# Optimization experiments

Hardware: AMD Instinct MI355X
Metric: run time of the kernel (lower is better)

Reference implementation:

```python
import jax, jax.numpy as jnp
import numpy as np

N = 50000
E = 800000
D = 128
L = 2
EPS = 1e-12  # BatchNorm1d eps in the module
NEG_SLOPE = 0.2  # PyG GATConv default leaky_relu slope


def setup_inputs() -> dict:
    key = jax.random.key(0)
    ks = jax.random.split(key, 12)
    x = jax.random.normal(ks[0], (N, D), dtype=jnp.float32)
    # edges guaranteed non-self (GATConv removes then re-adds self loops)
    src = jax.random.randint(ks[1], (E,), 0, N)
    off = jax.random.randint(ks[2], (E,), 1, N)
    dst = (src + off) % N
    edge_index = jnp.stack([src, dst]).astype(jnp.int64)
    scale = 1.0 / np.sqrt(D)
    Ws = jax.random.normal(ks[3], (L, D, D), dtype=jnp.float32) * scale
    a_src = jax.random.normal(ks[4], (L, D), dtype=jnp.float32) * scale
    a_dst = jax.random.normal(ks[5], (L, D), dtype=jnp.float32) * scale
    bias = jax.random.normal(ks[6], (L, D), dtype=jnp.float32) * 0.01
    gamma = jnp.ones((L, D), dtype=jnp.float32)
    beta = jnp.zeros((L, D), dtype=jnp.float32)
    run_mean = jax.random.normal(ks[7], (L, D), dtype=jnp.float32) * 0.01
    run_var = jax.random.uniform(ks[8], (L, D), minval=0.5, maxval=1.5, dtype=jnp.float32)
    return {"x": x, "edge_index": edge_index, "Ws": Ws, "a_src": a_src,
            "a_dst": a_dst, "bias": bias, "gamma": gamma, "beta": beta,
            "run_mean": run_mean, "run_var": run_var}


def _gat_layer(x, src, dst, W, asrc, adst, b):
    # x: [N, d_in]; W: [d_in, D]
    h = x @ W  # [N, D]
    e = jnp.take(h @ asrc, src) + jnp.take(h @ adst, dst)  # [E'] per-edge score
    e = jnp.where(e > 0, e, NEG_SLOPE * e)  # leaky_relu
    # segment softmax over destination node
    m = jax.ops.segment_max(e, dst, num_segments=N)
    ee = jnp.exp(e - jnp.take(m, dst))
    s = jax.ops.segment_sum(ee, dst, num_segments=N)
    alpha = ee / jnp.take(s, dst)
    # scatter-aggregate weighted source features
    msg = alpha[:, None] * jnp.take(h, src, axis=0)  # [E', D]
    out = jax.ops.segment_sum(msg, dst, num_segments=N)
    return out + b


def reference(x, edge_index, Ws, a_src, a_dst, bias, gamma, beta, run_mean, run_var):
    src, dst = edge_index[0], edge_index[1]
    # GATConv add_self_loops=True
    loops = jnp.arange(N, dtype=src.dtype)
    src = jnp.concatenate([src, loops])
    dst = jnp.concatenate([dst, loops])
    for i in range(L):
        x = _gat_layer(x, src, dst, Ws[i], a_src[i], a_dst[i], bias[i])
        # BatchNorm1d (eval mode, running stats) + ReLU
        x = (x - run_mean[i]) * (gamma[i] * jax.lax.rsqrt(run_var[i] + EPS)) + beta[i]
        x = jax.nn.relu(x)
    return x
```

## Files before the change

kernel.cpp:

```cpp
#include <hip/hip_runtime.h>

constexpr int Dd = 128;
constexpr float BN_EPS = 1e-12f;
constexpr float NEG_SLOPE = 0.2f;

using bf16x8 = __attribute__((ext_vector_type(8))) short;
using f32x4  = __attribute__((ext_vector_type(4))) float;

__device__ __forceinline__ ushort f2bf(float f) {
    unsigned u = __float_as_uint(f);
    return (ushort)((u + 0x7fffu + ((u >> 16) & 1u)) >> 16);
}
__device__ __forceinline__ float lrelu(float x) { return x > 0.f ? x : NEG_SLOPE * x; }

__global__ __launch_bounds__(256) void wprep_zero_kernel(
    const float* __restrict__ W, ushort* __restrict__ Wt, int* __restrict__ cntc,
    const float* __restrict__ bias, const float* __restrict__ gamma,
    const float* __restrict__ beta, const float* __restrict__ mean,
    const float* __restrict__ var, float* __restrict__ kA, float* __restrict__ kB)
{
    int t = threadIdx.x;
    if (blockIdx.x >= 2) {
        cntc[t] = 0;
        float sc = gamma[t] * rsqrtf(var[t] + BN_EPS);
        kA[t] = sc;
        kB[t] = (bias[t] - mean[t]) * sc + beta[t];
        return;
    }
    __shared__ float lds[32][33];
    const float* Wl = W + (size_t)blockIdx.x * Dd * Dd;
    ushort* Wo = Wt + (size_t)blockIdx.x * Dd * Dd;
    int r = t >> 3, c4 = (t & 7) << 2;
    for (int tk = 0; tk < 4; ++tk)
    for (int tn = 0; tn < 4; ++tn) {
        int k0 = tk * 32, n0 = tn * 32;
        float4 v = *(const float4*)&Wl[(size_t)(k0 + r) * Dd + n0 + c4];
        lds[r][c4] = v.x; lds[r][c4 + 1] = v.y; lds[r][c4 + 2] = v.z; lds[r][c4 + 3] = v.w;
        __syncthreads();
        ushort4 o;
        o.x = f2bf(lds[c4 + 0][r]); o.y = f2bf(lds[c4 + 1][r]);
        o.z = f2bf(lds[c4 + 2][r]); o.w = f2bf(lds[c4 + 3][r]);
        *(ushort4*)&Wo[(size_t)(n0 + r) * Dd + k0 + c4] = o;
        __syncthreads();
    }
}

__global__ __launch_bounds__(256) void coarse_hist_kernel(
    const int* __restrict__ dst, int* __restrict__ cntc, int E, int NB)
{
    __shared__ int lh[256];
    int t = threadIdx.x;
    lh[t] = 0;
    __syncthreads();
    for (int e = blockIdx.x * 256 + t; e < E; e += gridDim.x * 256)
        atomicAdd(&lh[dst[e] >> 8], 1);
    __syncthreads();
    if (t < NB && lh[t]) atomicAdd(&cntc[t], lh[t]);
}

__global__ __launch_bounds__(256) void coarse_scan_kernel(
    const int* __restrict__ cntc, int* __restrict__ base,
    int* __restrict__ cursor, int NB, int E)
{
    __shared__ int lds[256];
    int t = threadIdx.x;
    int v0 = (t < NB) ? cntc[t] : 0;
    lds[t] = v0;
    __syncthreads();
    for (int o = 1; o < 256; o <<= 1) {
        int v = (t >= o) ? lds[t - o] : 0;
        __syncthreads();
        lds[t] += v;
        __syncthreads();
    }
    int excl = lds[t] - v0;
    if (t < NB) { base[t] = excl; cursor[t] = excl; }
    if (t == 0) base[NB] = E;
}

__global__ __launch_bounds__(256) void partition_kernel(
    const int* __restrict__ src, const int* __restrict__ dst,
    int* __restrict__ cursor, unsigned* __restrict__ gpart, int E)
{
    __shared__ int h[256], lb[256], gs[256], cur[256];
    __shared__ unsigned staged[4096];
    const int t = threadIdx.x;
    const int c0 = blockIdx.x * 4096;
    const int count = min(4096, E - c0);

    h[t] = 0; cur[t] = 0;
    __syncthreads();
#pragma unroll
    for (int j = 0; j < 16; ++j) {
        int idx = j * 256 + t;
        if (idx < count) atomicAdd(&h[dst[c0 + idx] >> 8], 1);
    }
    __syncthreads();
    {
        int v0 = h[t];
        lb[t] = v0;
        __syncthreads();
        for (int o = 1; o < 256; o <<= 1) {
            int v = (t >= o) ? lb[t - o] : 0;
            __syncthreads();
            lb[t] += v;
            __syncthreads();
        }
        lb[t] -= v0;
    }
    if (h[t]) gs[t] = atomicAdd(&cursor[t], h[t]);
    __syncthreads();
#pragma unroll
    for (int j = 0; j < 16; ++j) {
        int idx = j * 256 + t;
        if (idx < count) {
            int d = dst[c0 + idx], s = src[c0 + idx];
            int b = d >> 8;
            int pos = lb[b] + atomicAdd(&cur[b], 1);
            staged[pos] = (unsigned)s | ((unsigned)(d & 255) << 16) | ((unsigned)b << 24);
        }
    }
    __syncthreads();
#pragma unroll
    for (int j = 0; j < 16; ++j) {
        int idx = j * 256 + t;
        if (idx < count) {
            unsigned p = staged[idx];
            int b = p >> 24;
            gpart[gs[b] + (idx - lb[b])] = p;
        }
    }
}

__global__ __launch_bounds__(256) void bucket_csr_kernel(
    const unsigned* __restrict__ gpart, const int* __restrict__ base,
    int* __restrict__ rowptr, int* __restrict__ ssrc, int N, int NB, int Etot)
{
    __shared__ int h[256], lb[256], cur[256];
    const int t = threadIdx.x;
    const int b = blockIdx.x;
    const int cb = base[b], ce = base[b + 1];
    const int cb2 = cb + b * 256;
    const int cnt = ce - cb;

    h[t] = 0; cur[t] = 0;
    __syncthreads();
    for (int o = t; o < cnt; o += 256)
        atomicAdd(&h[(gpart[cb + o] >> 16) & 255], 1);
    __syncthreads();
    {
        int v0 = h[t];
        lb[t] = v0;
        __syncthreads();
        for (int o = 1; o < 256; o <<= 1) {
            int v = (t >= o) ? lb[t - o] : 0;
            __syncthreads();
            lb[t] += v;
            __syncthreads();
        }
        lb[t] -= v0;
    }
    int n0 = b * 256 + t;
    if (n0 < N) {
        int rp = cb2 + lb[t] + t;
        rowptr[n0] = rp;
        ssrc[rp] = n0;
    }
    if (b == 0 && t == 0) rowptr[N] = Etot;
    __syncthreads();
    for (int o = t; o < cnt; o += 256) {
        unsigned p = gpart[cb + o];
        int n = (p >> 16) & 255;
        int pos = lb[n] + atomicAdd(&cur[n], 1);
        ssrc[cb2 + pos + n + 1] = (int)(p & 0xFFFFu);
    }
}

template<bool BF16IN>
__global__ __launch_bounds__(256) void gemm_mfma(
    const void* __restrict__ Xv, const ushort* __restrict__ Wt,
    const float* __restrict__ asrc, const float* __restrict__ adst,
    _Float16* __restrict__ Hf, float* __restrict__ hs, float* __restrict__ hd, int N)
{
    __shared__ ushort Xs[64 * 128];
    __shared__ ushort Bs[128 * 128];

    const int t = threadIdx.x;
    const int lane = t & 63, wid = t >> 6;
    const int row0 = blockIdx.x * 64;

    if constexpr (BF16IN) {
        const ushort* X = (const ushort*)Xv;
#pragma unroll
        for (int p = 0; p < 4; ++p) {
            int id = t + p * 256;
            int r = id >> 4, b16 = id & 15;
            int g = row0 + r;
            uint4 v = make_uint4(0, 0, 0, 0);
            if (g < N) v = *(const uint4*)&X[(size_t)g * Dd + b16 * 8];
            *(uint4*)&Xs[r * 128 + ((b16 ^ (r & 15)) << 3)] = v;
        }
    } else {
        const float* X = (const float*)Xv;
#pragma unroll
        for (int p = 0; p < 8; ++p) {
            int id = t + p * 256;
            int r = id >> 5, c4g = id & 31;
            int g = row0 + r;
            float4 v = make_float4(0.f, 0.f, 0.f, 0.f);
            if (g < N) v = *(const float4*)&X[(size_t)g * Dd + c4g * 4];
            ushort4 o; o.x = f2bf(v.x); o.y = f2bf(v.y); o.z = f2bf(v.z); o.w = f2bf(v.w);
            int b16 = c4g >> 1, sub = c4g & 1;
            *(ushort4*)&Xs[r * 128 + (((b16 ^ (r & 15)) << 3) | (sub << 2))] = o;
        }
    }
#pragma unroll
    for (int p = 0; p < 8; ++p) {
        int id = t + p * 256;
        int n = id >> 4, b16 = id & 15;
        uint4 v = *(const uint4*)&Wt[(size_t)n * 128 + b16 * 8];
        *(uint4*)&Bs[n * 128 + ((b16 ^ (n & 15)) << 3)] = v;
    }
    __syncthreads();

    f32x4 acc[8];
#pragma unroll
    for (int f = 0; f < 8; ++f) acc[f] = (f32x4){0.f, 0.f, 0.f, 0.f};

#pragma unroll
    for (int kk = 0; kk < 4; ++kk) {
        int ra = wid * 16 + (lane & 15);
        int b16 = (lane >> 4) + kk * 4;
        bf16x8 a = *(bf16x8*)&Xs[ra * 128 + ((b16 ^ (ra & 15)) << 3)];
#pragma unroll
        for (int f = 0; f < 8; ++f) {
            int nb = f * 16 + (lane & 15);
            bf16x8 b = *(bf16x8*)&Bs[nb * 128 + ((b16 ^ (nb & 15)) << 3)];
            acc[f] = __builtin_amdgcn_mfma_f32_16x16x32_bf16(a, b, acc[f], 0, 0, 0);
        }
    }

    float aS[8], aD[8];
#pragma unroll
    for (int f = 0; f < 8; ++f) {
        aS[f] = asrc[(lane & 15) + f * 16];
        aD[f] = adst[(lane & 15) + f * 16];
    }
#pragma unroll
    for (int j = 0; j < 4; ++j) {
        int r = row0 + wid * 16 + (lane >> 4) * 4 + j;
        float ps = 0.f, pd = 0.f;
#pragma unroll
        for (int f = 0; f < 8; ++f) { ps += acc[f][j] * aS[f]; pd += acc[f][j] * aD[f]; }
#pragma unroll
        for (int o = 8; o; o >>= 1) { ps += __shfl_xor(ps, o); pd += __shfl_xor(pd, o); }
        if (r < N) {
#pragma unroll
            for (int f = 0; f < 8; ++f)
                Hf[(size_t)r * Dd + (lane & 15) + f * 16] = (_Float16)acc[f][j];
            if ((lane & 15) == 0) { hs[r] = ps; hd[r] = pd; }
        }
    }
}

template<bool BF16OUT>
__global__ __launch_bounds__(256) void gat_agg_kernel(
    const int* __restrict__ rowptr, const int* __restrict__ ssrc,
    const float* __restrict__ hs, const float* __restrict__ hd,
    const _Float16* __restrict__ Hf,
    const float* __restrict__ kA, const float* __restrict__ kB,
    void* __restrict__ outv, int N)
{
    const int wid = (blockIdx.x * 256 + threadIdx.x) >> 6;
    if (wid >= N) return;
    const int lane = threadIdx.x & 63;
    const int q = lane >> 4, li = lane & 15;
    const size_t rowO = (size_t)wid * Dd;

    const float hdi = hd[wid];
    float acc[8];
#pragma unroll
    for (int m = 0; m < 8; ++m) acc[m] = 0.f;
    float s = 0.f;

    const int rs = rowptr[wid];
    const int nv = rowptr[wid + 1] - rs;

    union HU { uint4 u; _Float16 h[8]; };
    HU r0, r1; r0.u = make_uint4(0,0,0,0); r1.u = make_uint4(0,0,0,0);
    float h0 = 0.f, h1 = 0.f;
    if (q < nv) {
        int sj = ssrc[rs + q];
        h0 = hs[sj];
        r0.u = *(const uint4*)&Hf[(size_t)sj * Dd + li * 8];
    }
    if (4 + q < nv) {
        int sj = ssrc[rs + 4 + q];
        h1 = hs[sj];
        r1.u = *(const uint4*)&Hf[(size_t)sj * Dd + li * 8];
    }

    const int nit = (nv + 3) >> 2;
    for (int it = 0; it < nit; ++it) {
        float scv = h0 + hdi;
        scv = scv > 0.f ? scv : NEG_SLOPE * scv;
        float ee = (it * 4 + q < nv) ? __expf(scv) : 0.f;
        s += ee;
        HU rc = r0;
        r0 = r1; h0 = h1;
        int pn = (it + 2) * 4 + q;
        if (pn < nv) {
            int sj = ssrc[rs + pn];
            h1 = hs[sj];
            r1.u = *(const uint4*)&Hf[(size_t)sj * Dd + li * 8];
        }
#pragma unroll
        for (int m = 0; m < 8; ++m)
            acc[m] = fmaf((float)rc.h[m], ee, acc[m]);
    }

#pragma unroll
    for (int m = 0; m < 8; ++m) {
        acc[m] += __shfl_xor(acc[m], 16);
        acc[m] += __shfl_xor(acc[m], 32);
    }
    s += __shfl_xor(s, 16);
    s += __shfl_xor(s, 32);

    if (q == 0) {
        float inv = 1.0f / s;
        int c0 = li * 8;
        float4 ka0 = *(const float4*)&kA[c0],     ka1 = *(const float4*)&kA[c0 + 4];
        float4 kb0 = *(const float4*)&kB[c0],     kb1 = *(const float4*)&kB[c0 + 4];
        float o[8];
        o[0] = fmaxf(acc[0] * inv * ka0.x + kb0.x, 0.f);
        o[1] = fmaxf(acc[1] * inv * ka0.y + kb0.y, 0.f);
        o[2] = fmaxf(acc[2] * inv * ka0.z + kb0.z, 0.f);
        o[3] = fmaxf(acc[3] * inv * ka0.w + kb0.w, 0.f);
        o[4] = fmaxf(acc[4] * inv * ka1.x + kb1.x, 0.f);
        o[5] = fmaxf(acc[5] * inv * ka1.y + kb1.y, 0.f);
        o[6] = fmaxf(acc[6] * inv * ka1.z + kb1.z, 0.f);
        o[7] = fmaxf(acc[7] * inv * ka1.w + kb1.w, 0.f);
        if constexpr (BF16OUT) {
            ushort* out = (ushort*)outv;
            uint4 pk;
#pragma unroll
            for (int k = 0; k < 4; ++k)
                ((unsigned*)&pk)[k] = (unsigned)f2bf(o[2 * k]) | ((unsigned)f2bf(o[2 * k + 1]) << 16);
            *(uint4*)&out[rowO + c0] = pk;
        } else {
            float* out = (float*)outv;
            *(float4*)&out[rowO + c0]     = make_float4(o[0], o[1], o[2], o[3]);
            *(float4*)&out[rowO + c0 + 4] = make_float4(o[4], o[5], o[6], o[7]);
        }
    }
}

extern "C" void kernel_launch(void* const* d_in, const int* in_sizes, int n_in,
                              void* d_out, int out_size, void* d_ws, size_t ws_size,
                              hipStream_t stream)
{
    const float* x     = (const float*)d_in[0];
    const int*   ei    = (const int*)d_in[1];
    const float* Ws    = (const float*)d_in[2];
    const float* a_src = (const float*)d_in[3];
    const float* a_dst = (const float*)d_in[4];
    const float* bias  = (const float*)d_in[5];
    const float* gamma = (const float*)d_in[6];
    const float* beta  = (const float*)d_in[7];
    const float* mean  = (const float*)d_in[8];
    const float* var   = (const float*)d_in[9];
    float* out = (float*)d_out;
    float* ws  = (float*)d_ws;

    const int N = in_sizes[0] / Dd;
    const int E = in_sizes[1] / 2;
    const int Etot = E + N;
    const int NB = (N + 255) >> 8;
    const int* src = ei;
    const int* dst = ei + E;

    float*    hs   = ws;
    float*    hd   = hs + N;
    _Float16* Hf   = (_Float16*)(hd + N);
    ushort*   xmid = (ushort*)(Hf + (size_t)N * Dd);
    ushort*   WtB  = xmid + (size_t)N * Dd;
    float*    kAB  = (float*)(WtB + 2 * Dd * Dd);
    int* rowptr  = (int*)(kAB + 512);
    int* cntc    = rowptr + (N + 1);
    int* base    = cntc + 256;
    int* cursor  = base + 257;
    unsigned* gpart = (unsigned*)(cursor + 256);
    int* ssrc    = (int*)(gpart + E);

    const int gemm_blocks = (N + 63) / 64;
    const int part_blocks = (E + 4095) / 4096;
    const int agg_blocks  = (N * 64 + 255) / 256;

    wprep_zero_kernel<<<3, 256, 0, stream>>>(Ws, WtB, cntc, bias, gamma, beta, mean, var,
                                             kAB, kAB + 256);
    coarse_hist_kernel<<<256, 256, 0, stream>>>(dst, cntc, E, NB);
    coarse_scan_kernel<<<1, 256, 0, stream>>>(cntc, base, cursor, NB, E);
    partition_kernel<<<part_blocks, 256, 0, stream>>>(src, dst, cursor, gpart, E);
    bucket_csr_kernel<<<NB, 256, 0, stream>>>(gpart, base, rowptr, ssrc, N, NB, Etot);

    for (int l = 0; l < 2; ++l) {
        const float* kA_l = kAB + l * 128;
        const float* kB_l = kAB + 256 + l * 128;

        if (l == 0)
            gemm_mfma<false><<<gemm_blocks, 256, 0, stream>>>(
                (const void*)x, WtB, a_src, a_dst, Hf, hs, hd, N);
        else
            gemm_mfma<true><<<gemm_blocks, 256, 0, stream>>>(
                (const void*)xmid, WtB + (size_t)Dd * Dd, a_src + Dd, a_dst + Dd, Hf, hs, hd, N);

        if (l == 0)
            gat_agg_kernel<true><<<agg_blocks, 256, 0, stream>>>(
                rowptr, ssrc, hs, hd, Hf, kA_l, kB_l, (void*)xmid, N);
        else
            gat_agg_kernel<false><<<agg_blocks, 256, 0, stream>>>(
                rowptr, ssrc, hs, hd, Hf, kA_l, kB_l, (void*)out, N);
    }
}
```

Baseline: 242.7 us.

## Fuse layer-0 GEMM with degree histogram and deepen aggregation prefetch

The coarse destination histogram now runs as extra blocks of the layer-0 GEMM launch. This removes one kernel launch and lets the histogram overlap with the GEMM, since neither depends on the other. The aggregation loop now prefetches four neighbor groups ahead instead of two, via an unrolled rotating-register macro, to hide gather latency. The cost is more registers per thread, which may lower occupancy.

```diff
diff --git a/kernel.cpp b/kernel.cpp
--- a/kernel.cpp
+++ b/kernel.cpp
@@ -45,19 +45,6 @@
     }
 }
 
-__global__ __launch_bounds__(256) void coarse_hist_kernel(
-    const int* __restrict__ dst, int* __restrict__ cntc, int E, int NB)
-{
-    __shared__ int lh[256];
-    int t = threadIdx.x;
-    lh[t] = 0;
-    __syncthreads();
-    for (int e = blockIdx.x * 256 + t; e < E; e += gridDim.x * 256)
-        atomicAdd(&lh[dst[e] >> 8], 1);
-    __syncthreads();
-    if (t < NB && lh[t]) atomicAdd(&cntc[t], lh[t]);
-}
-
 __global__ __launch_bounds__(256) void coarse_scan_kernel(
     const int* __restrict__ cntc, int* __restrict__ base,
     int* __restrict__ cursor, int NB, int E)
@@ -176,9 +163,92 @@
     }
 }
 
-template<bool BF16IN>
-__global__ __launch_bounds__(256) void gemm_mfma(
-    const void* __restrict__ Xv, const ushort* __restrict__ Wt,
+__global__ __launch_bounds__(256) void gemm0_hist_kernel(
+    const float* __restrict__ X, const ushort* __restrict__ Wt,
+    const float* __restrict__ asrc, const float* __restrict__ adst,
+    _Float16* __restrict__ Hf, float* __restrict__ hs, float* __restrict__ hd, int N,
+    int nGemm, const int* __restrict__ dst, int* __restrict__ cntc, int E, int NB)
+{
+    const int t = threadIdx.x;
+    if (blockIdx.x >= nGemm) {
+        __shared__ int lh[256];
+        lh[t] = 0;
+        __syncthreads();
+        const int nb = 256;
+        for (int e = (blockIdx.x - nGemm) * 256 + t; e < E; e += nb * 256)
+            atomicAdd(&lh[dst[e] >> 8], 1);
+        __syncthreads();
+        if (t < NB && lh[t]) atomicAdd(&cntc[t], lh[t]);
+        return;
+    }
+
+    __shared__ ushort Xs[64 * 128];
+    __shared__ ushort Bs[128 * 128];
+    const int lane = t & 63, wid = t >> 6;
+    const int row0 = blockIdx.x * 64;
+
+#pragma unroll
+    for (int p = 0; p < 8; ++p) {
+        int id = t + p * 256;
+        int r = id >> 5, c4g = id & 31;
+        int g = row0 + r;
+        float4 v = make_float4(0.f, 0.f, 0.f, 0.f);
+        if (g < N) v = *(const float4*)&X[(size_t)g * Dd + c4g * 4];
+        ushort4 o; o.x = f2bf(v.x); o.y = f2bf(v.y); o.z = f2bf(v.z); o.w = f2bf(v.w);
+        int b16 = c4g >> 1, sub = c4g & 1;
+        *(ushort4*)&Xs[r * 128 + (((b16 ^ (r & 15)) << 3) | (sub << 2))] = o;
+    }
+#pragma unroll
+    for (int p = 0; p < 8; ++p) {
+        int id = t + p * 256;
+        int n = id >> 4, b16 = id & 15;
+        uint4 v = *(const uint4*)&Wt[(size_t)n * 128 + b16 * 8];
+        *(uint4*)&Bs[n * 128 + ((b16 ^ (n & 15)) << 3)] = v;
+    }
+    __syncthreads();
+
+    f32x4 acc[8];
+#pragma unroll
+    for (int f = 0; f < 8; ++f) acc[f] = (f32x4){0.f, 0.f, 0.f, 0.f};
+
+#pragma unroll
+    for (int kk = 0; kk < 4; ++kk) {
+        int ra = wid * 16 + (lane & 15);
+        int b16 = (lane >> 4) + kk * 4;
+        bf16x8 a = *(bf16x8*)&Xs[ra * 128 + ((b16 ^ (ra & 15)) << 3)];
+#pragma unroll
+        for (int f = 0; f < 8; ++f) {
+            int nb2 = f * 16 + (lane & 15);
+            bf16x8 b = *(bf16x8*)&Bs[nb2 * 128 + ((b16 ^ (nb2 & 15)) << 3)];
+            acc[f] = __builtin_amdgcn_mfma_f32_16x16x32_bf16(a, b, acc[f], 0, 0, 0);
+        }
+    }
+
+    float aS[8], aD[8];
+#pragma unroll
+    for (int f = 0; f < 8; ++f) {
+        aS[f] = asrc[(lane & 15) + f * 16];
+        aD[f] = adst[(lane & 15) + f * 16];
+    }
+#pragma unroll
+    for (int j = 0; j < 4; ++j) {
+        int r = row0 + wid * 16 + (lane >> 4) * 4 + j;
+        float ps = 0.f, pd = 0.f;
+#pragma unroll
+        for (int f = 0; f < 8; ++f) { ps += acc[f][j] * aS[f]; pd += acc[f][j] * aD[f]; }
+#pragma unroll
+        for (int o = 8; o; o >>= 1) { ps += __shfl_xor(ps, o); pd += __shfl_xor(pd, o); }
+        if (r < N) {
+#pragma unroll
+            for (int f = 0; f < 8; ++f)
+                Hf[(size_t)r * Dd + (lane & 15) + f * 16] = (_Float16)acc[f][j];
+            if ((lane & 15) == 0) { hs[r] = ps; hd[r] = pd; }
+        }
+    }
+}
+
+__global__ __launch_bounds__(256) void gemm_mfma_bf16(
+    const ushort* __restrict__ X, const ushort* __restrict__ Wt,
     const float* __restrict__ asrc, const float* __restrict__ adst,
     _Float16* __restrict__ Hf, float* __restrict__ hs, float* __restrict__ hd, int N)
 {
@@ -189,30 +259,14 @@
     const int lane = t & 63, wid = t >> 6;
     const int row0 = blockIdx.x * 64;
 
-    if constexpr (BF16IN) {
-        const ushort* X = (const ushort*)Xv;
-#pragma unroll
-        for (int p = 0; p < 4; ++p) {
-            int id = t + p * 256;
-            int r = id >> 4, b16 = id & 15;
-            int g = row0 + r;
-            uint4 v = make_uint4(0, 0, 0, 0);
-            if (g < N) v = *(const uint4*)&X[(size_t)g * Dd + b16 * 8];
-            *(uint4*)&Xs[r * 128 + ((b16 ^ (r & 15)) << 3)] = v;
-        }
-    } else {
-        const float* X = (const float*)Xv;
-#pragma unroll
-        for (int p = 0; p < 8; ++p) {
-            int id = t + p * 256;
-            int r = id >> 5, c4g = id & 31;
-            int g = row0 + r;
-            float4 v = make_float4(0.f, 0.f, 0.f, 0.f);
-            if (g < N) v = *(const float4*)&X[(size_t)g * Dd + c4g * 4];
-            ushort4 o; o.x = f2bf(v.x); o.y = f2bf(v.y); o.z = f2bf(v.z); o.w = f2bf(v.w);
-            int b16 = c4g >> 1, sub = c4g & 1;
-            *(ushort4*)&Xs[r * 128 + (((b16 ^ (r & 15)) << 3) | (sub << 2))] = o;
-        }
+#pragma unroll
+    for (int p = 0; p < 4; ++p) {
+        int id = t + p * 256;
+        int r = id >> 4, b16 = id & 15;
+        int g = row0 + r;
+        uint4 v = make_uint4(0, 0, 0, 0);
+        if (g < N) v = *(const uint4*)&X[(size_t)g * Dd + b16 * 8];
+        *(uint4*)&Xs[r * 128 + ((b16 ^ (r & 15)) << 3)] = v;
     }
 #pragma unroll
     for (int p = 0; p < 8; ++p) {
@@ -287,37 +341,45 @@
     const int nv = rowptr[wid + 1] - rs;
 
     union HU { uint4 u; _Float16 h[8]; };
-    HU r0, r1; r0.u = make_uint4(0,0,0,0); r1.u = make_uint4(0,0,0,0);
-    float h0 = 0.f, h1 = 0.f;
-    if (q < nv) {
-        int sj = ssrc[rs + q];
-        h0 = hs[sj];
-        r0.u = *(const uint4*)&Hf[(size_t)sj * Dd + li * 8];
-    }
-    if (4 + q < nv) {
-        int sj = ssrc[rs + 4 + q];
-        h1 = hs[sj];
-        r1.u = *(const uint4*)&Hf[(size_t)sj * Dd + li * 8];
-    }
+    HU r0, r1, r2, r3;
+    r0.u = r1.u = r2.u = r3.u = make_uint4(0, 0, 0, 0);
+    float h0 = 0.f, h1 = 0.f, h2 = 0.f, h3 = 0.f;
+
+    if (q < nv)      { int sj = ssrc[rs + q];      h0 = hs[sj]; r0.u = *(const uint4*)&Hf[(size_t)sj * Dd + li * 8]; }
+    if (4 + q < nv)  { int sj = ssrc[rs + 4 + q];  h1 = hs[sj]; r1.u = *(const uint4*)&Hf[(size_t)sj * Dd + li * 8]; }
+    if (8 + q < nv)  { int sj = ssrc[rs + 8 + q];  h2 = hs[sj]; r2.u = *(const uint4*)&Hf[(size_t)sj * Dd + li * 8]; }
+    if (12 + q < nv) { int sj = ssrc[rs + 12 + q]; h3 = hs[sj]; r3.u = *(const uint4*)&Hf[(size_t)sj * Dd + li * 8]; }
 
     const int nit = (nv + 3) >> 2;
-    for (int it = 0; it < nit; ++it) {
-        float scv = h0 + hdi;
-        scv = scv > 0.f ? scv : NEG_SLOPE * scv;
-        float ee = (it * 4 + q < nv) ? __expf(scv) : 0.f;
-        s += ee;
-        HU rc = r0;
-        r0 = r1; h0 = h1;
-        int pn = (it + 2) * 4 + q;
-        if (pn < nv) {
-            int sj = ssrc[rs + pn];
-            h1 = hs[sj];
-            r1.u = *(const uint4*)&Hf[(size_t)sj * Dd + li * 8];
-        }
-#pragma unroll
-        for (int m = 0; m < 8; ++m)
-            acc[m] = fmaf((float)rc.h[m], ee, acc[m]);
-    }
+
+#define AGG_STEP(RK, HK)                                                 \
+    {                                                                    \
+             \
+        int pn = (it + 4) * 4 + q;                                       \
+        uint4 tn = RK.u; float th = HK;                                  \
+        if (pn < nv) {                                                   \
+            int sj = ssrc[rs + pn];                                      \
+            th = hs[sj];                                                 \
+            tn = *(const uint4*)&Hf[(size_t)sj * Dd + li * 8];           \
+        }                                                                \
+        float scv = HK + hdi;                                            \
+        scv = scv > 0.f ? scv : NEG_SLOPE * scv;                         \
+        float ee = (it * 4 + q < nv) ? __expf(scv) : 0.f;                \
+        s += ee;                                                         \
+        _Pragma("unroll")                                                \
+        for (int m = 0; m < 8; ++m)                                      \
+            acc[m] = fmaf((float)RK.h[m], ee, acc[m]);                   \
+        RK.u = tn; HK = th;                                              \
+    }
+
+    int it = 0;
+    while (true) {
+        AGG_STEP(r0, h0); if (++it >= nit) break;
+        AGG_STEP(r1, h1); if (++it >= nit) break;
+        AGG_STEP(r2, h2); if (++it >= nit) break;
+        AGG_STEP(r3, h3); if (++it >= nit) break;
+    }
+#undef AGG_STEP
 
 #pragma unroll
     for (int m = 0; m < 8; ++m) {
@@ -399,27 +461,17 @@
 
     wprep_zero_kernel<<<3, 256, 0, stream>>>(Ws, WtB, cntc, bias, gamma, beta, mean, var,
                                              kAB, kAB + 256);
-    coarse_hist_kernel<<<256, 256, 0, stream>>>(dst, cntc, E, NB);
+    gemm0_hist_kernel<<<gemm_blocks + 256, 256, 0, stream>>>(
+        x, WtB, a_src, a_dst, Hf, hs, hd, N, gemm_blocks, dst, cntc, E, NB);
     coarse_scan_kernel<<<1, 256, 0, stream>>>(cntc, base, cursor, NB, E);
     partition_kernel<<<part_blocks, 256, 0, stream>>>(src, dst, cursor, gpart, E);
     bucket_csr_kernel<<<NB, 256, 0, stream>>>(gpart, base, rowptr, ssrc, N, NB, Etot);
 
-    for (int l = 0; l < 2; ++l) {
-        const float* kA_l = kAB + l * 128;
-        const float* kB_l = kAB + 256 + l * 128;
-
-        if (l == 0)
-            gemm_mfma<false><<<gemm_blocks, 256, 0, stream>>>(
-                (const void*)x, WtB, a_src, a_dst, Hf, hs, hd, N);
-        else
-            gemm_mfma<true><<<gemm_blocks, 256, 0, stream>>>(
-                (const void*)xmid, WtB + (size_t)Dd * Dd, a_src + Dd, a_dst + Dd, Hf, hs, hd, N);
-
-        if (l == 0)
-            gat_agg_kernel<true><<<agg_blocks, 256, 0, stream>>>(
-                rowptr, ssrc, hs, hd, Hf, kA_l, kB_l, (void*)xmid, N);
-        else
-            gat_agg_kernel<false><<<agg_blocks, 256, 0, stream>>>(
-                rowptr, ssrc, hs, hd, Hf, kA_l, kB_l, (void*)out, N);
-    }
-}
+    gat_agg_kernel<true><<<agg_blocks, 256, 0, stream>>>(
+        rowptr, ssrc, hs, hd, Hf, kAB, kAB + 256, (void*)xmid, N);
+
+    gemm_mfma_bf16<<<gemm_blocks, 256, 0, stream>>>(
+        xmid, WtB + (size_t)Dd * Dd, a_src + Dd, a_dst + Dd, Hf, hs, hd, N);
+    gat_agg_kernel<false><<<agg_blocks, 256, 0, stream>>>(
+        rowptr, ssrc, hs, hd, Hf, kAB + 128, kAB + 256 + 128, (void*)out, N);
+}
```

Result: slower. 283.8 us (+16.9%).
